# Performance work log

Hardware: AMD Instinct MI355X
Metric: run time of the kernel (lower is better)

The kernel has to match this reference:

```python
import jax, jax.numpy as jnp
import numpy as np

EPS = 1e-6
NUM_HEADS = 8
ATTN_DIM = 64
LINEAR_DIM = 64


def _layer_norm(x, eps=EPS):
    # F.layer_norm without elementwise affine
    mu = jnp.mean(x, axis=-1, keepdims=True)
    var = jnp.mean(jnp.square(x - mu), axis=-1, keepdims=True)
    return (x - mu) * jax.lax.rsqrt(var + eps)


def setup_inputs() -> dict:
    key = jax.random.key(0)
    k1, k2, k3 = jax.random.split(key, 3)
    B, N, D = 4, 2048, 512
    x = jax.random.normal(k1, (B, N, D), dtype=jnp.float32)
    invalid_attn_mask = jnp.tril(jnp.ones((N, N), dtype=jnp.float32))  # causal
    uvqk = jax.random.normal(k2, (D, 2 * LINEAR_DIM * NUM_HEADS + 2 * ATTN_DIM * NUM_HEADS), dtype=jnp.float32) * 0.02
    o_w = jax.random.normal(k3, (D, LINEAR_DIM * NUM_HEADS), dtype=jnp.float32) * (1.0 / np.sqrt(D))  # torch Linear weight [out, in]
    o_b = jnp.zeros((D,), dtype=jnp.float32)
    return {"x": x, "invalid_attn_mask": invalid_attn_mask, "uvqk": uvqk, "o_w": o_w, "o_b": o_b}


def reference(x, invalid_attn_mask, uvqk, o_w, o_b):
    B, N, D = x.shape
    H, dA, dL = NUM_HEADS, ATTN_DIM, LINEAR_DIM
    normed_x = _layer_norm(x)
    # fused uvqk projection + silu activation
    proj = jax.nn.silu(jnp.einsum('bnd,de->bne', normed_x, uvqk))
    u, v, q, k = jnp.split(proj, [dL * H, 2 * dL * H, 2 * dL * H + dA * H], axis=-1)
    q_h = q.reshape(B, N, H, dA)
    k_h = k.reshape(B, N, H, dA)
    v_h = v.reshape(B, N, H, dL)
    # HSTU attention: SiLU(qk)/N, then mask multiply (no softmax)
    qk_attn = jnp.einsum('bnhd,bmhd->bhnm', q_h, k_h)
    qk_attn = jax.nn.silu(qk_attn) / N
    qk_attn = qk_attn * invalid_attn_mask[None, None, :, :]
    attn = jnp.einsum('bhnm,bmhd->bnhd', qk_attn, v_h).reshape(B, N, H * dL)
    a = _layer_norm(attn)
    o_input = u * a
    out = jnp.einsum('bnf,df->bnd', o_input, o_w) + o_b + x
    return out
```

## Files before the change

### kernel.cpp

```cpp
#include <hip/hip_runtime.h>
#include <cstdint>

#define NTOK 2048
#define DIM 512
#define EDIM 2048
#define BATCH 4
#define HEADS 8
#define BNROWS 8192
#define INV_N (1.0f/2048.0f)

typedef unsigned short u16;
typedef __bf16 bf16x8 __attribute__((ext_vector_type(8)));
typedef u16   u16x8  __attribute__((ext_vector_type(8)));
typedef u16   u16x4  __attribute__((ext_vector_type(4)));
typedef float f32x4  __attribute__((ext_vector_type(4)));

__device__ __forceinline__ u16 f2bf(float f) {
  union { float f; uint32_t u; } v; v.f = f;
  uint32_t r = v.u + 0x7FFFu + ((v.u >> 16) & 1u);
  return (u16)(r >> 16);
}
__device__ __forceinline__ u16 f2bfc(float f) {
  return __builtin_bit_cast(u16, (__bf16)f);
}
__device__ __forceinline__ float bf2f(u16 b) {
  union { uint32_t u; float f; } v; v.u = ((uint32_t)b) << 16;
  return v.f;
}
__device__ __forceinline__ bf16x8 ldb(const u16* p) {
  u16x8 r = *(const u16x8*)p;
  return __builtin_bit_cast(bf16x8, r);
}
#define MFMA16(a,b,c) __builtin_amdgcn_mfma_f32_16x16x32_bf16((a),(b),(c),0,0,0)

__device__ __forceinline__ float silu_nr(float s) {
  float e = __expf(-s);
  e = fminf(e, 1.7e38f);
  float d = 1.0f + e;
  float r = __builtin_amdgcn_rcpf(d);
  r = r * fmaf(-d, r, 2.0f);
  return s * r;
}

__device__ __forceinline__ void gload16(const u16* g, u16* lds) {
  __builtin_amdgcn_global_load_lds(
      (const __attribute__((address_space(1))) void*)g,
      (__attribute__((address_space(3))) void*)lds, 16, 0, 0);
}

__global__ __launch_bounds__(256) void k_pre(const float* __restrict__ uvqk,
                                             const float* __restrict__ ow,
                                             const float* __restrict__ x,
                                             u16* __restrict__ uvqk_t,
                                             u16* __restrict__ ow_bf,
                                             u16* __restrict__ xn) {
  __shared__ float tile[32][33];
  int bid = blockIdx.x, tid = threadIdx.x;
  if (bid < 1024) {
    int tx = tid & 31, ty = tid >> 5;
    int j0 = (bid & 63) * 32, k0 = (bid >> 6) * 32;
#pragma unroll
    for (int r = ty; r < 32; r += 8)
      tile[r][tx] = uvqk[(size_t)(k0 + r) * EDIM + j0 + tx];
    __syncthreads();
#pragma unroll
    for (int r = ty; r < 32; r += 8)
      uvqk_t[(size_t)(j0 + r) * DIM + k0 + tx] = f2bfc(tile[tx][r]);
  } else if (bid < 1280) {
    int i4 = (bid - 1024) * 1024 + tid * 4;
    float4 v = *(const float4*)(ow + i4);
    u16x4 o = {f2bfc(v.x), f2bfc(v.y), f2bfc(v.z), f2bfc(v.w)};
    *(u16x4*)(ow_bf + i4) = o;
  } else {
    int lane = tid & 63, wid = tid >> 6;
    size_t row = (size_t)(bid - 1280) * 4 + wid;
    const float* xr = x + row * DIM;
    float4 a = ((const float4*)xr)[lane * 2];
    float4 b = ((const float4*)xr)[lane * 2 + 1];
    float s = a.x + a.y + a.z + a.w + b.x + b.y + b.z + b.w;
#pragma unroll
    for (int o = 32; o; o >>= 1) s += __shfl_xor(s, o);
    float mu = s * (1.0f / DIM);
    float d[8] = {a.x - mu, a.y - mu, a.z - mu, a.w - mu,
                  b.x - mu, b.y - mu, b.z - mu, b.w - mu};
    float v = 0.f;
#pragma unroll
    for (int j = 0; j < 8; ++j) v += d[j] * d[j];
#pragma unroll
    for (int o = 32; o; o >>= 1) v += __shfl_xor(v, o);
    float rs = rsqrtf(v * (1.0f / DIM) + 1e-6f);
    u16x8 o8;
#pragma unroll
    for (int j = 0; j < 8; ++j) o8[j] = f2bfc(d[j] * rs);
    *(u16x8*)(xn + row * DIM + lane * 8) = o8;
  }
}

__global__ __launch_bounds__(256) void k_gemm1(const u16* __restrict__ A,
                                               const u16* __restrict__ Bt,
                                               u16* __restrict__ P,
                                               u16* __restrict__ vt) {
  __shared__ u16 As[128 * 64];
  __shared__ u16 Bs[128 * 64];
  int tid = threadIdx.x, lane = tid & 63, wid = tid >> 6;
  int lm = lane & 15, lg = lane >> 4;
  int wr = wid >> 1, wc = wid & 1;

  int bid = blockIdx.x;
  int xcd = bid & 7, idx = bid >> 3;
  int orig = xcd * 128 + idx;
  int r0 = (orig >> 4) * 128;
  int c0 = (orig & 15) * 128;

  int srow = wid * 8 + (lane >> 3);
  int scol = ((lane & 7) ^ (lane >> 3)) * 8;

  f32x4 acc[4][4];
  f32x4 z = {0.f, 0.f, 0.f, 0.f};
#pragma unroll
  for (int mt = 0; mt < 4; ++mt)
#pragma unroll
    for (int nt = 0; nt < 4; ++nt) acc[mt][nt] = z;

  int ksw = (lm & 7) << 3;

  for (int ks = 0; ks < DIM / 64; ++ks) {
#pragma unroll
    for (int it = 0; it < 4; ++it) {
      gload16(A + (size_t)(r0 + it * 32 + srow) * DIM + ks * 64 + scol,
              As + it * 2048 + wid * 512);
      gload16(Bt + (size_t)(c0 + it * 32 + srow) * DIM + ks * 64 + scol,
              Bs + it * 2048 + wid * 512);
    }
    __syncthreads();

#pragma unroll
    for (int kk = 0; kk < 2; ++kk) {
      bf16x8 am[4], bn[4];
#pragma unroll
      for (int mt = 0; mt < 4; ++mt)
        am[mt] = ldb(&As[(wr * 64 + mt * 16 + lm) * 64 + ((kk * 32 + lg * 8) ^ ksw)]);
#pragma unroll
      for (int nt = 0; nt < 4; ++nt)
        bn[nt] = ldb(&Bs[(wc * 64 + nt * 16 + lm) * 64 + ((kk * 32 + lg * 8) ^ ksw)]);
#pragma unroll
      for (int mt = 0; mt < 4; ++mt)
#pragma unroll
        for (int nt = 0; nt < 4; ++nt)
          acc[mt][nt] = MFMA16(am[mt], bn[nt], acc[mt][nt]);
    }
    __syncthreads();
  }

  bool isv = (c0 >= 512) && (c0 < 1024);
  int btc = r0 >> 11;
  int nbw = (r0 & 2047) + wr * 64;
  int hv  = ((c0 - 512) >> 6) + wc;

  u16* ws = ((wid >> 1) ? Bs : As) + (wid & 1) * 4096;

#pragma unroll
  for (int mt = 0; mt < 4; ++mt)
#pragma unroll
    for (int nt = 0; nt < 4; ++nt) {
      u16 pv[4];
#pragma unroll
      for (int i = 0; i < 4; ++i)
        pv[i] = f2bfc(silu_nr(acc[mt][nt][i]));
      if (isv) {
        int e = nt * 16 + lm;
        int n = nbw + mt * 16 + lg * 4;
        u16x4 pk = {pv[0], pv[1], pv[2], pv[3]};
        *(u16x4*)(vt + ((size_t)(btc * 8 + hv) * 64 + e) * NTOK + n) = pk;
      } else {
#pragma unroll
        for (int i = 0; i < 4; ++i) {
          int row = mt * 16 + lg * 4 + i;
          int col = nt * 16 + lm;
          ws[row * 64 + (col ^ ((row & 7) << 3))] = pv[i];
        }
      }
    }

  if (!isv) {
#pragma unroll
    for (int p = 0; p < 8; ++p) {
      int rrow = p * 8 + (lane >> 3);
      int rcol = (lane & 7) * 8;
      u16x8 vv = *(const u16x8*)&ws[rrow * 64 + (rcol ^ ((rrow & 7) << 3))];
      *(u16x8*)(P + (size_t)(r0 + wr * 64 + rrow) * EDIM + c0 + wc * 64 + rcol) = vv;
    }
  }
}

__global__ __launch_bounds__(256) void k_attn(const u16* __restrict__ proj,
                                              const u16* __restrict__ vt,
                                              u16* __restrict__ attnb) {
  __shared__ u16 kv0[8192];
  __shared__ u16 kv1[8192];
  __shared__ u16 p_lds[4][16][64];
  int tid = threadIdx.x, lane = tid & 63, w = tid >> 6;
  int lm = lane & 15, lg = lane >> 4;

  int bid = blockIdx.x;
  int xcd = bid & 7, idx = bid >> 3;
  int j = idx >> 2, pj = j & 7;
  int qtile = (j < 8) ? (31 - pj) : (j < 16) ? (16 + pj)
                      : (j < 24) ? (15 - pj) : pj;
  int bh = (xcd << 2) + (idx & 3);
  int b = bh >> 3, h = bh & 7;
  int n0 = qtile * 64;
  int nrow = n0 + w * 16;
  int nlm = nrow + lm;

  const u16* pb = proj + (size_t)b * NTOK * EDIM;
  const u16* kb = pb + 1536 + h * 64;
  const u16* vb = vt + (size_t)bh * 64 * NTOK;

  f32x4 z = {0.f, 0.f, 0.f, 0.f};

  int sr = lane >> 3;
  int sc = ((lane & 7) ^ sr) * 8;
  const u16* ks0 = kb + (size_t)(w * 16 + sr) * EDIM + sc;
  const u16* ks1 = kb + (size_t)(w * 16 + 8 + sr) * EDIM + sc;
  const u16* vs0 = vb + (size_t)(w * 16 + sr) * NTOK + sc;
  const u16* vs1 = vb + (size_t)(w * 16 + 8 + sr) * NTOK + sc;

  const u16* qrow = pb + (size_t)nlm * EDIM + 1024 + h * 64 + lg * 8;
  bf16x8 qf0 = ldb(qrow), qf1 = ldb(qrow + 32);

  f32x4 acc[4];
#pragma unroll
  for (int et = 0; et < 4; ++et) acc[et] = z;

  int psw = (lm & 7) << 3;

  gload16(ks0, kv0 + (w * 16) * 64);
  gload16(ks1, kv0 + (w * 16 + 8) * 64);
  gload16(vs0, kv0 + 4096 + (w * 16) * 64);
  gload16(vs1, kv0 + 4096 + (w * 16 + 8) * 64);
  asm volatile("s_waitcnt vmcnt(0)" ::: "memory");
  __builtin_amdgcn_s_barrier();

  int ntl = qtile + 1;
  for (int t = 0; t < ntl; ++t) {
    const u16* kt = (t & 1) ? kv1 : kv0;
    const u16* vl = kt + 4096;
    if (t + 1 < ntl) {
      u16* kd = ((t + 1) & 1) ? kv1 : kv0;
      size_t ko = (size_t)(t + 1) * 64 * EDIM;
      size_t vo = (size_t)(t + 1) * 64;
      gload16(ks0 + ko, kd + (w * 16) * 64);
      gload16(ks1 + ko, kd + (w * 16 + 8) * 64);
      gload16(vs0 + vo, kd + 4096 + (w * 16) * 64);
      gload16(vs1 + vo, kd + 4096 + (w * 16 + 8) * 64);
    }
    bf16x8 kf[4][2];
#pragma unroll
    for (int mb = 0; mb < 4; ++mb)
#pragma unroll
      for (int kk = 0; kk < 2; ++kk)
        kf[mb][kk] = ldb(&kt[(mb * 16 + lm) * 64 +
                             ((kk * 32 + lg * 8) ^ ((lm & 7) << 3))]);
    if (t == qtile) {
#pragma unroll
      for (int mb = 0; mb < 4; ++mb) {
        f32x4 s = MFMA16(kf[mb][0], qf0, z);
        s = MFMA16(kf[mb][1], qf1, s);
        int m = t * 64 + mb * 16 + lg * 4;
        u16x4 pk;
#pragma unroll
        for (int i = 0; i < 4; ++i)
          pk[i] = (m + i <= nlm) ? f2bfc(silu_nr(s[i])) : (u16)0;
        *(u16x4*)&p_lds[w][lm][(mb * 16 + lg * 4) ^ psw] = pk;
      }
    } else {
#pragma unroll
      for (int mb = 0; mb < 4; ++mb) {
        f32x4 s = MFMA16(kf[mb][0], qf0, z);
        s = MFMA16(kf[mb][1], qf1, s);
        u16x4 pk;
#pragma unroll
        for (int i = 0; i < 4; ++i) pk[i] = f2bfc(silu_nr(s[i]));
        *(u16x4*)&p_lds[w][lm][(mb * 16 + lg * 4) ^ psw] = pk;
      }
    }
    bf16x8 vf[2][4];
#pragma unroll
    for (int kk = 0; kk < 2; ++kk)
#pragma unroll
      for (int et = 0; et < 4; ++et)
        vf[kk][et] = ldb(&vl[(et * 16 + lm) * 64 +
                             ((kk * 32 + lg * 8) ^ ((lm & 7) << 3))]);
    bf16x8 pf0 = ldb(&p_lds[w][lm][(lg * 8) ^ psw]);
    bf16x8 pf1 = ldb(&p_lds[w][lm][(32 + lg * 8) ^ psw]);
#pragma unroll
    for (int et = 0; et < 4; ++et) {
      acc[et] = MFMA16(pf0, vf[0][et], acc[et]);
      acc[et] = MFMA16(pf1, vf[1][et], acc[et]);
    }
    asm volatile("s_waitcnt vmcnt(0)" ::: "memory");
    __builtin_amdgcn_s_barrier();
  }

#pragma unroll
  for (int et = 0; et < 4; ++et)
#pragma unroll
    for (int i = 0; i < 4; ++i)
      attnb[((size_t)b * NTOK + nrow + lg * 4 + i) * DIM +
            h * 64 + et * 16 + lm] = f2bfc(acc[et][i] * INV_N);
}

__global__ __launch_bounds__(256) void k_gemm2f(const u16* __restrict__ attnb,
                                                const u16* __restrict__ proj,
                                                const u16* __restrict__ Bw,
                                                const float* __restrict__ o_b,
                                                const float* __restrict__ x,
                                                float* __restrict__ out) {
  __shared__ u16 os[32 * 512];
  int tid = threadIdx.x, lane = tid & 63, w = tid >> 6;
  int lm = lane & 15, lg = lane >> 4;

  int bid = blockIdx.x;
  int xcd = bid & 7, idx = bid >> 3;
  int r0 = (xcd * 32 + idx) * 32;

#pragma unroll
  for (int rr = 0; rr < 8; ++rr) {
    int r = w * 8 + rr;
    u16x8 a8 = *(const u16x8*)(attnb + (size_t)(r0 + r) * DIM + lane * 8);
    float av[8];
#pragma unroll
    for (int j = 0; j < 8; ++j) av[j] = bf2f(a8[j]);
    float s = av[0] + av[1] + av[2] + av[3] + av[4] + av[5] + av[6] + av[7];
#pragma unroll
    for (int o = 32; o; o >>= 1) s += __shfl_xor(s, o);
    float mu = s * (1.0f / DIM);
    float d[8];
#pragma unroll
    for (int j = 0; j < 8; ++j) d[j] = av[j] - mu;
    float v = 0.f;
#pragma unroll
    for (int j = 0; j < 8; ++j) v += d[j] * d[j];
#pragma unroll
    for (int o = 32; o; o >>= 1) v += __shfl_xor(v, o);
    float rs = rsqrtf(v * (1.0f / DIM) + 1e-6f);
    u16x8 u8 = *(const u16x8*)(proj + (size_t)(r0 + r) * EDIM + lane * 8);
    u16x8 o8;
#pragma unroll
    for (int j = 0; j < 8; ++j) o8[j] = f2bfc(bf2f(u8[j]) * (d[j] * rs));
    *(u16x8*)&os[r * 512 + ((lane * 8) ^ ((r & 7) << 3))] = o8;
  }
  __syncthreads();

  int cb = w * 128;
  f32x4 acc[2][8];
  f32x4 z = {0.f, 0.f, 0.f, 0.f};
#pragma unroll
  for (int mt = 0; mt < 2; ++mt)
#pragma unroll
    for (int nt = 0; nt < 8; ++nt) acc[mt][nt] = z;

#pragma unroll 2
  for (int kc = 0; kc < 16; ++kc) {
    bf16x8 af[2];
#pragma unroll
    for (int mt = 0; mt < 2; ++mt)
      af[mt] = ldb(&os[(mt * 16 + lm) * 512 +
                       ((kc * 32 + lg * 8) ^ ((lm & 7) << 3))]);
    bf16x8 bfr[8];
#pragma unroll
    for (int nt = 0; nt < 8; ++nt)
      bfr[nt] = ldb(Bw + (size_t)(cb + nt * 16 + lm) * DIM + kc * 32 + lg * 8);
#pragma unroll
    for (int mt = 0; mt < 2; ++mt)
#pragma unroll
      for (int nt = 0; nt < 8; ++nt)
        acc[mt][nt] = MFMA16(af[mt], bfr[nt], acc[mt][nt]);
  }

#pragma unroll
  for (int mt = 0; mt < 2; ++mt)
#pragma unroll
    for (int nt = 0; nt < 8; ++nt)
#pragma unroll
      for (int i = 0; i < 4; ++i) {
        size_t row = r0 + mt * 16 + lg * 4 + i;
        int col = cb + nt * 16 + lm;
        out[row * DIM + col] = acc[mt][nt][i] + o_b[col] + x[row * DIM + col];
      }
}

extern "C" void kernel_launch(void* const* d_in, const int* in_sizes, int n_in,
                              void* d_out, int out_size, void* d_ws, size_t ws_size,
                              hipStream_t stream) {
  const float* x    = (const float*)d_in[0];
  const float* uvqk = (const float*)d_in[2];
  const float* o_w  = (const float*)d_in[3];
  const float* o_b  = (const float*)d_in[4];
  float* out = (float*)d_out;

  u16* uvqk_t = (u16*)d_ws;
  u16* ow_bf  = uvqk_t + (size_t)EDIM * DIM;
  u16* xn     = ow_bf + (size_t)DIM * DIM;
  u16* proj   = xn + (size_t)BNROWS * DIM;
  u16* attnb  = proj + (size_t)BNROWS * EDIM;
  u16* vt     = attnb + (size_t)BNROWS * DIM;

  k_pre<<<dim3(3328), 256, 0, stream>>>(uvqk, o_w, x, uvqk_t, ow_bf, xn);
  k_gemm1<<<dim3(1024), 256, 0, stream>>>(xn, uvqk_t, proj, vt);
  k_attn<<<dim3(1024), 256, 0, stream>>>(proj, vt, attnb);
  k_gemm2f<<<dim3(256), 256, 0, stream>>>(attnb, proj, ow_bf, o_b, x, out);
}
```

Before: 102.0 us.

## Widen gemm1 tile to 128x256 and store epilogue directly to global

Doubles the N extent of each k_gemm1 block to 256 columns, so each wave computes a 64x128 sub-tile and A-tile loads are reused across twice as many columns, halving the grid to 512 blocks. The LDS-staged, swizzled epilogue for the non-V outputs is replaced by direct scalar 2-byte stores to P. Larger accumulators raise register pressure (launch_bounds asks for 2 blocks/SM), and the scalar strided stores may coalesce worse than the previous 16-byte row writes.

```diff
diff --git a/kernel.cpp b/kernel.cpp
--- a/kernel.cpp
+++ b/kernel.cpp
@@ -96,57 +96,57 @@
   }
 }
 
-__global__ __launch_bounds__(256) void k_gemm1(const u16* __restrict__ A,
-                                               const u16* __restrict__ Bt,
-                                               u16* __restrict__ P,
-                                               u16* __restrict__ vt) {
+__global__ __launch_bounds__(256, 2) void k_gemm1(const u16* __restrict__ A,
+                                                  const u16* __restrict__ Bt,
+                                                  u16* __restrict__ P,
+                                                  u16* __restrict__ vt) {
   __shared__ u16 As[128 * 64];
-  __shared__ u16 Bs[128 * 64];
+  __shared__ u16 Bs[256 * 64];
   int tid = threadIdx.x, lane = tid & 63, wid = tid >> 6;
   int lm = lane & 15, lg = lane >> 4;
   int wr = wid >> 1, wc = wid & 1;
 
   int bid = blockIdx.x;
   int xcd = bid & 7, idx = bid >> 3;
-  int orig = xcd * 128 + idx;
-  int r0 = (orig >> 4) * 128;
-  int c0 = (orig & 15) * 128;
-
-  int srow = wid * 8 + (lane >> 3);
+  int r0 = (xcd * 8 + (idx >> 3)) * 128;
+  int c0 = (idx & 7) * 256;
+
+  int srow = tid >> 3;
   int scol = ((lane & 7) ^ (lane >> 3)) * 8;
 
-  f32x4 acc[4][4];
+  f32x4 acc[4][8];
   f32x4 z = {0.f, 0.f, 0.f, 0.f};
 #pragma unroll
   for (int mt = 0; mt < 4; ++mt)
 #pragma unroll
-    for (int nt = 0; nt < 4; ++nt) acc[mt][nt] = z;
+    for (int nt = 0; nt < 8; ++nt) acc[mt][nt] = z;
 
   int ksw = (lm & 7) << 3;
 
   for (int ks = 0; ks < DIM / 64; ++ks) {
 #pragma unroll
-    for (int it = 0; it < 4; ++it) {
+    for (int it = 0; it < 4; ++it)
       gload16(A + (size_t)(r0 + it * 32 + srow) * DIM + ks * 64 + scol,
               As + it * 2048 + wid * 512);
+#pragma unroll
+    for (int it = 0; it < 8; ++it)
       gload16(Bt + (size_t)(c0 + it * 32 + srow) * DIM + ks * 64 + scol,
               Bs + it * 2048 + wid * 512);
-    }
     __syncthreads();
 
 #pragma unroll
     for (int kk = 0; kk < 2; ++kk) {
-      bf16x8 am[4], bn[4];
+      bf16x8 am[4], bn[8];
 #pragma unroll
       for (int mt = 0; mt < 4; ++mt)
         am[mt] = ldb(&As[(wr * 64 + mt * 16 + lm) * 64 + ((kk * 32 + lg * 8) ^ ksw)]);
 #pragma unroll
-      for (int nt = 0; nt < 4; ++nt)
-        bn[nt] = ldb(&Bs[(wc * 64 + nt * 16 + lm) * 64 + ((kk * 32 + lg * 8) ^ ksw)]);
+      for (int nt = 0; nt < 8; ++nt)
+        bn[nt] = ldb(&Bs[(wc * 128 + nt * 16 + lm) * 64 + ((kk * 32 + lg * 8) ^ ksw)]);
 #pragma unroll
       for (int mt = 0; mt < 4; ++mt)
 #pragma unroll
-        for (int nt = 0; nt < 4; ++nt)
+        for (int nt = 0; nt < 8; ++nt)
           acc[mt][nt] = MFMA16(am[mt], bn[nt], acc[mt][nt]);
     }
     __syncthreads();
@@ -155,42 +155,31 @@
   bool isv = (c0 >= 512) && (c0 < 1024);
   int btc = r0 >> 11;
   int nbw = (r0 & 2047) + wr * 64;
-  int hv  = ((c0 - 512) >> 6) + wc;
-
-  u16* ws = ((wid >> 1) ? Bs : As) + (wid & 1) * 4096;
+  int cw = c0 + wc * 128;
 
 #pragma unroll
   for (int mt = 0; mt < 4; ++mt)
 #pragma unroll
-    for (int nt = 0; nt < 4; ++nt) {
+    for (int nt = 0; nt < 8; ++nt) {
       u16 pv[4];
 #pragma unroll
       for (int i = 0; i < 4; ++i)
         pv[i] = f2bfc(silu_nr(acc[mt][nt][i]));
       if (isv) {
-        int e = nt * 16 + lm;
+        int hv = (cw + nt * 16 - 512) >> 6;
+        int e = (nt & 3) * 16 + lm;
         int n = nbw + mt * 16 + lg * 4;
         u16x4 pk = {pv[0], pv[1], pv[2], pv[3]};
         *(u16x4*)(vt + ((size_t)(btc * 8 + hv) * 64 + e) * NTOK + n) = pk;
       } else {
+        int col = cw + nt * 16 + lm;
 #pragma unroll
         for (int i = 0; i < 4; ++i) {
-          int row = mt * 16 + lg * 4 + i;
-          int col = nt * 16 + lm;
-          ws[row * 64 + (col ^ ((row & 7) << 3))] = pv[i];
+          size_t row = r0 + wr * 64 + mt * 16 + lg * 4 + i;
+          P[row * EDIM + col] = pv[i];
         }
       }
     }
-
-  if (!isv) {
-#pragma unroll
-    for (int p = 0; p < 8; ++p) {
-      int rrow = p * 8 + (lane >> 3);
-      int rcol = (lane & 7) * 8;
-      u16x8 vv = *(const u16x8*)&ws[rrow * 64 + (rcol ^ ((rrow & 7) << 3))];
-      *(u16x8*)(P + (size_t)(r0 + wr * 64 + rrow) * EDIM + c0 + wc * 64 + rcol) = vv;
-    }
-  }
 }
 
 __global__ __launch_bounds__(256) void k_attn(const u16* __restrict__ proj,
@@ -408,7 +397,7 @@
   u16* vt     = attnb + (size_t)BNROWS * DIM;
 
   k_pre<<<dim3(3328), 256, 0, stream>>>(uvqk, o_w, x, uvqk_t, ow_bf, xn);
-  k_gemm1<<<dim3(1024), 256, 0, stream>>>(xn, uvqk_t, proj, vt);
+  k_gemm1<<<dim3(512), 256, 0, stream>>>(xn, uvqk_t, proj, vt);
   k_attn<<<dim3(1024), 256, 0, stream>>>(proj, vt, attnb);
   k_gemm2f<<<dim3(256), 256, 0, stream>>>(attnb, proj, ow_bf, o_b, x, out);
 }
```

Measured after the change: 97.37 us (median of 2 runs). -4.5%, faster.
